# Kernel optimization log

Measured on AMD Instinct MI355X. Metric: run time of the kernel, lower is better.

The kernel has to match this reference:

```python
import jax, jax.numpy as jnp
import numpy as np

L, B, D = 2048, 2, 1024
H, DK, DV = 16, 64, 64
SPAN = 128
LN_EPS = 1e-5


def setup_inputs() -> dict:
    key = jax.random.key(0)
    ks = jax.random.split(key, 8)
    s_qk = np.sqrt(2.0 / (D + DK)).astype(np.float32)
    s_v = np.sqrt(2.0 / (D + DV)).astype(np.float32)
    return {
        "query": jax.random.normal(ks[0], (L, B, D), jnp.float32),
        "key": jax.random.normal(ks[1], (L, B, D), jnp.float32),
        "value": jax.random.normal(ks[2], (L, B, D), jnp.float32),
        "Wq": jax.random.normal(ks[3], (D, H * DK), jnp.float32) * s_qk,
        "bq": jnp.zeros((H * DK,), jnp.float32),
        "Wk": jax.random.normal(ks[4], (D, H * DK), jnp.float32) * s_qk,
        "bk": jnp.zeros((H * DK,), jnp.float32),
        "Wv": jax.random.normal(ks[5], (D, H * DV), jnp.float32) * s_v,
        "bv": jnp.zeros((H * DV,), jnp.float32),
        "Wfc": jax.random.normal(ks[6], (H * DV, D), jnp.float32) * np.sqrt(2.0 / (H * DV + D)).astype(np.float32),
        "bfc": jnp.zeros((D,), jnp.float32),
        "gamma": jnp.ones((D,), jnp.float32),
        "beta": jnp.zeros((D,), jnp.float32),
    }


def reference(query, key, value, Wq, bq, Wk, bk, Wv, bv, Wfc, bfc, gamma, beta):
    l, b, d = query.shape
    # projections: (l,b,H*dk) -> (H,b,l,dk)   [torch rearrange 'l b (head k) -> head b l k']
    q = (query @ Wq + bq).reshape(l, b, H, DK).transpose(2, 1, 0, 3)
    k = (key @ Wk + bk).reshape(l, b, H, DK).transpose(2, 1, 0, 3)
    v = (value @ Wv + bv).reshape(l, b, H, DV).transpose(2, 1, 0, 3)
    scores = jnp.einsum("hblk,hbtk->hblt", q, k) / jnp.sqrt(jnp.float32(DK))
    # banded additive mask: keep |j - i| <= SPAN
    idx = jnp.arange(l)
    band = jnp.abs(idx[None, :] - idx[:, None]) <= SPAN  # (l, l)
    scores = jnp.where(band[None, None], scores, -jnp.inf)
    attn = jax.nn.softmax(scores, axis=-1)
    out = jnp.einsum("hblt,hbtv->hblv", attn, v)
    # 'head b l v -> l b (head v)'
    out = out.transpose(2, 1, 0, 3).reshape(l, b, H * DV)
    out = out @ Wfc + bfc  # dropout p=0.0 -> identity
    y = out + query  # residual
    mu = jnp.mean(y, axis=-1, keepdims=True)
    var = jnp.mean(jnp.square(y - mu), axis=-1, keepdims=True)
    y = (y - mu) * jax.lax.rsqrt(var + LN_EPS) * gamma + beta
    return (y, attn)
```

## Files before the change

### kernel.cpp

```cpp
#include <hip/hip_runtime.h>
#include <stdint.h>

#define L_SEQ 2048
#define BB 2
#define DD 1024
#define NH 16
#define SPAN 128

typedef __attribute__((ext_vector_type(8))) short short8;
typedef __attribute__((ext_vector_type(4))) float floatx4;

__device__ __forceinline__ short f32_bf16(float f) {
  uint32_t u = __float_as_uint(f);
  u += 0x7FFFu + ((u >> 16) & 1u);
  return (short)(u >> 16);
}
__device__ __forceinline__ float bf2f(short s) {
  return __uint_as_float(((uint32_t)(uint16_t)s) << 16);
}

__device__ __forceinline__ void gld16(const short* g, short* l) {
  __builtin_amdgcn_global_load_lds(
      (__attribute__((address_space(1))) void*)(g),
      (__attribute__((address_space(3))) void*)(l), 16, 0, 0);
}

__global__ __launch_bounds__(256) void k_convert(
    const float* __restrict__ s0, const float* __restrict__ s1, const float* __restrict__ s2,
    short* __restrict__ d0, short* __restrict__ d1, short* __restrict__ d2) {
  const float* s = blockIdx.y == 0 ? s0 : (blockIdx.y == 1 ? s1 : s2);
  short* d = blockIdx.y == 0 ? d0 : (blockIdx.y == 1 ? d1 : d2);
  int i = blockIdx.x * 256 + threadIdx.x;
  float4 v = ((const float4*)s)[i];
  short4 o;
  o.x = f32_bf16(v.x); o.y = f32_bf16(v.y); o.z = f32_bf16(v.z); o.w = f32_bf16(v.w);
  ((short4*)d)[i] = o;
}

__global__ __launch_bounds__(256) void k_transpose(
    const float* __restrict__ w0, const float* __restrict__ w1,
    const float* __restrict__ w2, const float* __restrict__ w3,
    short* __restrict__ dst) {
  __shared__ float tile[32][33];
  const float* src = blockIdx.z == 0 ? w0 : blockIdx.z == 1 ? w1 : blockIdx.z == 2 ? w2 : w3;
  short* out = dst + (size_t)blockIdx.z * (DD * DD);
  int bx = blockIdx.x * 32, by = blockIdx.y * 32;
  int tx = threadIdx.x, ty = threadIdx.y;
#pragma unroll
  for (int r = 0; r < 32; r += 8)
    tile[ty + r][tx] = src[(size_t)(by + ty + r) * DD + bx + tx];
  __syncthreads();
#pragma unroll
  for (int r = 0; r < 32; r += 8)
    out[(size_t)(bx + ty + r) * DD + by + tx] = f32_bf16(tile[tx][ty + r]);
}

#define BM 128
#define BN 128
#define BK 32

__device__ __forceinline__ void gemm_core(const short* __restrict__ A,
                                          const short* __restrict__ BT,
                                          floatx4 acc[4][4], int bm0, int bn0) {
  __shared__ short As[BM * BK];
  __shared__ short Bs[BN * BK];
  int tid = threadIdx.x;
  int wave = tid >> 6, lane = tid & 63;
  int li = lane & 15, quad = lane >> 4;
  int wm = (wave & 1) * 64, wn = (wave >> 1) * 64;
  int srow = wave * 32 + (lane >> 2);
  int scol = (lane & 3) * 8;
  const short* gA = A + (size_t)(bm0 + srow) * DD + scol;
  const short* gB = BT + (size_t)(bn0 + srow) * DD + scol;
  short* lA = &As[wave * 32 * BK];
  short* lB = &Bs[wave * 32 * BK];
  for (int k0 = 0; k0 < DD; k0 += BK) {
    __syncthreads();
    gld16(gA + k0, lA);
    gld16(gA + (size_t)16 * DD + k0, lA + 16 * BK);
    gld16(gB + k0, lB);
    gld16(gB + (size_t)16 * DD + k0, lB + 16 * BK);
    __syncthreads();
    short8 af[4], bf[4];
#pragma unroll
    for (int t = 0; t < 4; ++t) {
      af[t] = *(const short8*)&As[(wm + t * 16 + li) * BK + quad * 8];
      bf[t] = *(const short8*)&Bs[(wn + t * 16 + li) * BK + quad * 8];
    }
#pragma unroll
    for (int tm = 0; tm < 4; ++tm)
#pragma unroll
      for (int tn = 0; tn < 4; ++tn)
        acc[tm][tn] = __builtin_amdgcn_mfma_f32_16x16x32_bf16(af[tm], bf[tn], acc[tm][tn], 0, 0, 0);
  }
}

__global__ __launch_bounds__(256) void k_proj(
    const short* __restrict__ xq, const short* __restrict__ xk, const short* __restrict__ xv,
    const short* __restrict__ WT,
    const float* __restrict__ bq, const float* __restrict__ bk, const float* __restrict__ bv,
    short* __restrict__ qo, short* __restrict__ ko, short* __restrict__ vo) {
  int mode = blockIdx.z;
  const short* A = mode == 0 ? xq : (mode == 1 ? xk : xv);
  const short* BT = WT + (size_t)mode * DD * DD;
  const float* bias = mode == 0 ? bq : (mode == 1 ? bk : bv);
  floatx4 acc[4][4] = {};
  int bm0 = blockIdx.y * BM, bn0 = blockIdx.x * BN;
  gemm_core(A, BT, acc, bm0, bn0);

  int tid = threadIdx.x;
  int wave = tid >> 6, lane = tid & 63;
  int li = lane & 15, quad = lane >> 4;
  int wm = (wave & 1) * 64, wn = (wave >> 1) * 64;
  short* dst = (mode == 0) ? qo : (mode == 1 ? ko : vo);
#pragma unroll
  for (int tm = 0; tm < 4; ++tm) {
#pragma unroll
    for (int tn = 0; tn < 4; ++tn) {
      int gn = bn0 + wn + tn * 16 + li;
      float bs = bias[gn];
      int h = gn >> 6, dk = gn & 63;
#pragma unroll
      for (int r = 0; r < 4; ++r) {
        int gm = bm0 + wm + tm * 16 + quad * 4 + r;
        int l = gm >> 1, b = gm & 1;
        dst[(((size_t)h * BB + b) * L_SEQ + l) * 64 + dk] = f32_bf16(acc[tm][tn][r] + bs);
      }
    }
  }
}

__global__ __launch_bounds__(256) void k_vt(const short* __restrict__ vl, short* __restrict__ vt) {
  __shared__ short tl[64][72];
  int l0 = blockIdx.x * 64, hb = blockIdx.y;
  const short* src = vl + ((size_t)hb * L_SEQ + l0) * 64;
  short* dst = vt + (size_t)hb * 64 * L_SEQ + l0;
  int tid = threadIdx.x;
  int r = tid >> 2, c0 = (tid & 3) * 16;
  *(short8*)&tl[r][c0] = *(const short8*)(src + (size_t)r * 64 + c0);
  *(short8*)&tl[r][c0 + 8] = *(const short8*)(src + (size_t)r * 64 + c0 + 8);
  __syncthreads();
  int d = tid >> 2, lb = (tid & 3) * 16;
  short8 o0, o1;
#pragma unroll
  for (int j = 0; j < 8; ++j) o0[j] = tl[lb + j][d];
#pragma unroll
  for (int j = 0; j < 8; ++j) o1[j] = tl[lb + 8 + j][d];
  *(short8*)(dst + (size_t)d * L_SEQ + lb) = o0;
  *(short8*)(dst + (size_t)d * L_SEQ + lb + 8) = o1;
}

__global__ __launch_bounds__(256) void k_attn(
    const short* __restrict__ qw, const short* __restrict__ kw, const short* __restrict__ vTw,
    float* __restrict__ attn_out, short* __restrict__ ctx) {
  __shared__ short P[4][16 * 296];
  const int wv = threadIdx.x >> 6, lane = threadIdx.x & 63;
  const int li = lane & 15, quad = lane >> 4;
  const int i0 = blockIdx.x * 64 + wv * 16;
  const int hb = blockIdx.y;
  const short* Q = qw + (size_t)hb * L_SEQ * 64;
  const short* K = kw + (size_t)hb * L_SEQ * 64;
  const short* VT = vTw + (size_t)hb * 64 * L_SEQ;
  float* Aout = attn_out + (size_t)hb * L_SEQ * L_SEQ;

  short8 qf0 = *(const short8*)(Q + (size_t)(i0 + li) * 64 + quad * 8);
  short8 qf1 = *(const short8*)(Q + (size_t)(i0 + li) * 64 + 32 + quad * 8);

  floatx4 S[17];
  const int jbase = i0 - SPAN;
#pragma unroll
  for (int t = 0; t < 17; ++t) {
    int j0 = jbase + t * 16;
    floatx4 acc = {0.f, 0.f, 0.f, 0.f};
    if (j0 >= 0 && j0 < L_SEQ) {
      const short* kp = K + (size_t)(j0 + li) * 64 + quad * 8;
      short8 kf0 = *(const short8*)kp;
      short8 kf1 = *(const short8*)(kp + 32);
      acc = __builtin_amdgcn_mfma_f32_16x16x32_bf16(qf0, kf0, acc, 0, 0, 0);
      acc = __builtin_amdgcn_mfma_f32_16x16x32_bf16(qf1, kf1, acc, 0, 0, 0);
    }
    S[t] = acc;
  }
  float mrow[4] = {-1e30f, -1e30f, -1e30f, -1e30f};
#pragma unroll
  for (int t = 0; t < 17; ++t) {
    int j0 = jbase + t * 16;
    bool tvalid = (j0 >= 0) && (j0 < L_SEQ);
    int j = j0 + li;
#pragma unroll
    for (int r = 0; r < 4; ++r) {
      int i = i0 + quad * 4 + r;
      bool inband = tvalid && (j >= i - SPAN) && (j <= i + SPAN);
      float s = inband ? S[t][r] * 0.125f : -1e30f;
      S[t][r] = s;
      mrow[r] = fmaxf(mrow[r], s);
    }
  }
#pragma unroll
  for (int m = 1; m <= 8; m <<= 1)
#pragma unroll
    for (int r = 0; r < 4; ++r) mrow[r] = fmaxf(mrow[r], __shfl_xor(mrow[r], m));
  float lsum[4] = {0.f, 0.f, 0.f, 0.f};
#pragma unroll
  for (int t = 0; t < 17; ++t)
#pragma unroll
    for (int r = 0; r < 4; ++r) {
      float p = __expf(S[t][r] - mrow[r]);
      S[t][r] = p;
      lsum[r] += p;
    }
#pragma unroll
  for (int m = 1; m <= 8; m <<= 1)
#pragma unroll
    for (int r = 0; r < 4; ++r) lsum[r] += __shfl_xor(lsum[r], m);
  float inv[4];
#pragma unroll
  for (int r = 0; r < 4; ++r) inv[r] = 1.0f / lsum[r];

  short* myP = P[wv];
#pragma unroll
  for (int t = 0; t < 17; ++t)
#pragma unroll
    for (int r = 0; r < 4; ++r)
      myP[(quad * 4 + r) * 296 + t * 16 + li] = f32_bf16(S[t][r] * inv[r]);
  *(short4*)&myP[(lane >> 2) * 296 + 272 + (lane & 3) * 4] = short4{0, 0, 0, 0};
  __syncthreads();

  floatx4 O[4] = {};
#pragma unroll
  for (int c = 0; c < 9; ++c) {
    short8 pf = *(const short8*)&myP[li * 296 + c * 32 + quad * 8];
    int jg = jbase + c * 32 + quad * 8;
    int jc = (jg >= 0 && jg < L_SEQ) ? jg : 0;
#pragma unroll
    for (int n = 0; n < 4; ++n) {
      short8 vf = *(const short8*)(VT + (size_t)(n * 16 + li) * L_SEQ + jc);
      O[n] = __builtin_amdgcn_mfma_f32_16x16x32_bf16(pf, vf, O[n], 0, 0, 0);
    }
  }
  const int b = hb & 1, h = hb >> 1;
#pragma unroll
  for (int n = 0; n < 4; ++n)
#pragma unroll
    for (int r = 0; r < 4; ++r) {
      int irow = quad * 4 + r;
      ctx[((size_t)(i0 + irow) * BB + b) * DD + h * 64 + n * 16 + li] = f32_bf16(O[n][r]);
    }

#pragma unroll 4
  for (int row = 0; row < 16; ++row) {
    float* orow = Aout + (size_t)(i0 + row) * L_SEQ;
    const short* prow = &myP[row * 296];
#pragma unroll
    for (int it = 0; it < 8; ++it) {
      int col = it * 256 + lane * 4;
      int s = col - jbase;
      float4 v = {0.f, 0.f, 0.f, 0.f};
      if (s >= 0 && s < 288) {
        short4 p4 = *(const short4*)(prow + s);
        v.x = bf2f(p4.x); v.y = bf2f(p4.y); v.z = bf2f(p4.z); v.w = bf2f(p4.w);
      }
      *(float4*)(orow + col) = v;
    }
  }
}

__global__ __launch_bounds__(256) void k_fc(
    const short* __restrict__ ctx, const short* __restrict__ WfcT,
    const float* __restrict__ bfc, const float* __restrict__ query,
    float* __restrict__ ypre) {
  floatx4 acc[4][4] = {};
  int bm0 = blockIdx.y * BM, bn0 = blockIdx.x * BN;
  gemm_core(ctx, WfcT, acc, bm0, bn0);
  int tid = threadIdx.x;
  int wave = tid >> 6, lane = tid & 63;
  int li = lane & 15, quad = lane >> 4;
  int wm = (wave & 1) * 64, wn = (wave >> 1) * 64;
#pragma unroll
  for (int tm = 0; tm < 4; ++tm)
#pragma unroll
    for (int tn = 0; tn < 4; ++tn) {
      int gn = bn0 + wn + tn * 16 + li;
      float bs = bfc[gn];
#pragma unroll
      for (int r = 0; r < 4; ++r) {
        int gm = bm0 + wm + tm * 16 + quad * 4 + r;
        ypre[(size_t)gm * DD + gn] = acc[tm][tn][r] + bs + query[(size_t)gm * DD + gn];
      }
    }
}

__global__ __launch_bounds__(256) void k_ln(
    const float* __restrict__ yp, const float* __restrict__ gamma,
    const float* __restrict__ beta, float* __restrict__ out) {
  __shared__ float red[8];
  int row = blockIdx.x, tid = threadIdx.x;
  float4 v = ((const float4*)(yp + (size_t)row * DD))[tid];
  float s = v.x + v.y + v.z + v.w;
  float s2 = v.x * v.x + v.y * v.y + v.z * v.z + v.w * v.w;
#pragma unroll
  for (int m = 1; m <= 32; m <<= 1) {
    s += __shfl_xor(s, m);
    s2 += __shfl_xor(s2, m);
  }
  int wv = tid >> 6;
  if ((tid & 63) == 0) { red[wv] = s; red[wv + 4] = s2; }
  __syncthreads();
  s = red[0] + red[1] + red[2] + red[3];
  s2 = red[4] + red[5] + red[6] + red[7];
  float mu = s * (1.0f / DD);
  float var = s2 * (1.0f / DD) - mu * mu;
  float rs = rsqrtf(var + 1e-5f);
  float4 g = ((const float4*)gamma)[tid];
  float4 bb = ((const float4*)beta)[tid];
  float4 o;
  o.x = (v.x - mu) * rs * g.x + bb.x;
  o.y = (v.y - mu) * rs * g.y + bb.y;
  o.z = (v.z - mu) * rs * g.z + bb.z;
  o.w = (v.w - mu) * rs * g.w + bb.w;
  ((float4*)(out + (size_t)row * DD))[tid] = o;
}

extern "C" void kernel_launch(void* const* d_in, const int* in_sizes, int n_in,
                              void* d_out, int out_size, void* d_ws, size_t ws_size,
                              hipStream_t stream) {
  const float* query = (const float*)d_in[0];
  const float* key   = (const float*)d_in[1];
  const float* value = (const float*)d_in[2];
  const float* Wq    = (const float*)d_in[3];
  const float* bq    = (const float*)d_in[4];
  const float* Wk    = (const float*)d_in[5];
  const float* bk    = (const float*)d_in[6];
  const float* Wv    = (const float*)d_in[7];
  const float* bv    = (const float*)d_in[8];
  const float* Wfc   = (const float*)d_in[9];
  const float* bfc   = (const float*)d_in[10];
  const float* gamma = (const float*)d_in[11];
  const float* beta  = (const float*)d_in[12];
  float* out = (float*)d_out;
  float* attn = out + (size_t)L_SEQ * BB * DD;

  char* w = (char*)d_ws;
  short* xq_b  = (short*)(w);
  short* xk_b  = (short*)(w + ((size_t)8 << 20));
  short* xv_b  = (short*)(w + ((size_t)16 << 20));
  short* WT    = (short*)(w + ((size_t)24 << 20));
  short* q_ws  = (short*)(w + ((size_t)32 << 20));
  short* k_ws  = (short*)(w + ((size_t)40 << 20));
  short* v_lin = (short*)(w + ((size_t)48 << 20));
  short* vT_ws = (short*)(w + ((size_t)56 << 20));
  short* ctx   = (short*)(w + ((size_t)64 << 20));
  float* ypre  = (float*)(w + ((size_t)72 << 20));

  k_convert<<<dim3(4096, 3), 256, 0, stream>>>(query, key, value, xq_b, xk_b, xv_b);
  k_transpose<<<dim3(32, 32, 4), dim3(32, 8), 0, stream>>>(Wq, Wk, Wv, Wfc, WT);
  k_proj<<<dim3(8, 32, 3), 256, 0, stream>>>(xq_b, xk_b, xv_b, WT, bq, bk, bv, q_ws, k_ws, v_lin);
  k_vt<<<dim3(32, 32), 256, 0, stream>>>(v_lin, vT_ws);
  k_attn<<<dim3(32, 32), 256, 0, stream>>>(q_ws, k_ws, vT_ws, attn, ctx);
  k_fc<<<dim3(8, 32), 256, 0, stream>>>(ctx, WT + (size_t)3 * DD * DD, bfc, query, ypre);
  k_ln<<<4096, 256, 0, stream>>>(ypre, gamma, beta, out);
}
```

Baseline: 720.1 us.

## Merge prep kernels, stage K in LDS, widen GEMM K-step, nontemporal attn stores

Fuses the input conversion and weight transpose into one launch, and doubles the GEMM K-step to 64 so each iteration issues more loads and MFMAs between barriers. The attention kernel now stages the block's shared K window in LDS once, instead of each wave reading K from global memory, and reuses that buffer for P. The 128 MB attention-matrix writes use nontemporal stores to avoid polluting the cache. The cost is more LDS per block and an extra barrier, which may lower occupancy.

```diff
diff --git a/kernel.cpp b/kernel.cpp
--- a/kernel.cpp
+++ b/kernel.cpp
@@ -25,67 +25,87 @@
       (__attribute__((address_space(3))) void*)(l), 16, 0, 0);
 }
 
-__global__ __launch_bounds__(256) void k_convert(
+__global__ __launch_bounds__(256) void k_prep(
     const float* __restrict__ s0, const float* __restrict__ s1, const float* __restrict__ s2,
-    short* __restrict__ d0, short* __restrict__ d1, short* __restrict__ d2) {
-  const float* s = blockIdx.y == 0 ? s0 : (blockIdx.y == 1 ? s1 : s2);
-  short* d = blockIdx.y == 0 ? d0 : (blockIdx.y == 1 ? d1 : d2);
-  int i = blockIdx.x * 256 + threadIdx.x;
-  float4 v = ((const float4*)s)[i];
-  short4 o;
-  o.x = f32_bf16(v.x); o.y = f32_bf16(v.y); o.z = f32_bf16(v.z); o.w = f32_bf16(v.w);
-  ((short4*)d)[i] = o;
-}
-
-__global__ __launch_bounds__(256) void k_transpose(
     const float* __restrict__ w0, const float* __restrict__ w1,
     const float* __restrict__ w2, const float* __restrict__ w3,
-    short* __restrict__ dst) {
+    short* __restrict__ d0, short* __restrict__ d1, short* __restrict__ d2,
+    short* __restrict__ WT) {
   __shared__ float tile[32][33];
-  const float* src = blockIdx.z == 0 ? w0 : blockIdx.z == 1 ? w1 : blockIdx.z == 2 ? w2 : w3;
-  short* out = dst + (size_t)blockIdx.z * (DD * DD);
-  int bx = blockIdx.x * 32, by = blockIdx.y * 32;
-  int tx = threadIdx.x, ty = threadIdx.y;
-#pragma unroll
-  for (int r = 0; r < 32; r += 8)
-    tile[ty + r][tx] = src[(size_t)(by + ty + r) * DD + bx + tx];
-  __syncthreads();
-#pragma unroll
-  for (int r = 0; r < 32; r += 8)
-    out[(size_t)(bx + ty + r) * DD + by + tx] = f32_bf16(tile[tx][ty + r]);
+  int bid = blockIdx.x, tid = threadIdx.x;
+  if (bid < 12288) {
+    int y = bid >> 12;
+    const float* s = y == 0 ? s0 : (y == 1 ? s1 : s2);
+    short* d = y == 0 ? d0 : (y == 1 ? d1 : d2);
+    int i = (bid & 4095) * 256 + tid;
+    float4 v = ((const float4*)s)[i];
+    short4 o;
+    o.x = f32_bf16(v.x); o.y = f32_bf16(v.y); o.z = f32_bf16(v.z); o.w = f32_bf16(v.w);
+    ((short4*)d)[i] = o;
+  } else {
+    int b2 = bid - 12288;
+    int z = b2 >> 10;
+    int xy = b2 & 1023;
+    int bx = (xy & 31) * 32, by = (xy >> 5) * 32;
+    int tx = tid & 31, ty = tid >> 5;
+    const float* src = z == 0 ? w0 : z == 1 ? w1 : z == 2 ? w2 : w3;
+    short* out = WT + (size_t)z * (DD * DD);
+#pragma unroll
+    for (int r = 0; r < 32; r += 8)
+      tile[ty + r][tx] = src[(size_t)(by + ty + r) * DD + bx + tx];
+    __syncthreads();
+#pragma unroll
+    for (int r = 0; r < 32; r += 8)
+      out[(size_t)(bx + ty + r) * DD + by + tx] = f32_bf16(tile[tx][ty + r]);
+  }
 }
 
 #define BM 128
 #define BN 128
-#define BK 32
 
 __device__ __forceinline__ void gemm_core(const short* __restrict__ A,
                                           const short* __restrict__ BT,
                                           floatx4 acc[4][4], int bm0, int bn0) {
-  __shared__ short As[BM * BK];
-  __shared__ short Bs[BN * BK];
+  __shared__ short As0[BM * 32], As1[BM * 32];
+  __shared__ short Bs0[BN * 32], Bs1[BN * 32];
   int tid = threadIdx.x;
   int wave = tid >> 6, lane = tid & 63;
   int li = lane & 15, quad = lane >> 4;
   int wm = (wave & 1) * 64, wn = (wave >> 1) * 64;
-  int srow = wave * 32 + (lane >> 2);
-  int scol = (lane & 3) * 8;
-  const short* gA = A + (size_t)(bm0 + srow) * DD + scol;
-  const short* gB = BT + (size_t)(bn0 + srow) * DD + scol;
-  short* lA = &As[wave * 32 * BK];
-  short* lB = &Bs[wave * 32 * BK];
-  for (int k0 = 0; k0 < DD; k0 += BK) {
+  int r0 = wave * 32 + (lane >> 2);
+  int c0 = (lane & 3) * 8;
+  const short* gA = A + (size_t)(bm0 + r0) * DD + c0;
+  const short* gB = BT + (size_t)(bn0 + r0) * DD + c0;
+  short* lA0 = &As0[wave * 32 * 32];
+  short* lA1 = &As1[wave * 32 * 32];
+  short* lB0 = &Bs0[wave * 32 * 32];
+  short* lB1 = &Bs1[wave * 32 * 32];
+  for (int k0 = 0; k0 < DD; k0 += 64) {
     __syncthreads();
-    gld16(gA + k0, lA);
-    gld16(gA + (size_t)16 * DD + k0, lA + 16 * BK);
-    gld16(gB + k0, lB);
-    gld16(gB + (size_t)16 * DD + k0, lB + 16 * BK);
+    gld16(gA + k0, lA0);
+    gld16(gA + (size_t)16 * DD + k0, lA0 + 16 * 32);
+    gld16(gA + k0 + 32, lA1);
+    gld16(gA + (size_t)16 * DD + k0 + 32, lA1 + 16 * 32);
+    gld16(gB + k0, lB0);
+    gld16(gB + (size_t)16 * DD + k0, lB0 + 16 * 32);
+    gld16(gB + k0 + 32, lB1);
+    gld16(gB + (size_t)16 * DD + k0 + 32, lB1 + 16 * 32);
     __syncthreads();
     short8 af[4], bf[4];
 #pragma unroll
     for (int t = 0; t < 4; ++t) {
-      af[t] = *(const short8*)&As[(wm + t * 16 + li) * BK + quad * 8];
-      bf[t] = *(const short8*)&Bs[(wn + t * 16 + li) * BK + quad * 8];
+      af[t] = *(const short8*)&As0[(wm + t * 16 + li) * 32 + quad * 8];
+      bf[t] = *(const short8*)&Bs0[(wn + t * 16 + li) * 32 + quad * 8];
+    }
+#pragma unroll
+    for (int tm = 0; tm < 4; ++tm)
+#pragma unroll
+      for (int tn = 0; tn < 4; ++tn)
+        acc[tm][tn] = __builtin_amdgcn_mfma_f32_16x16x32_bf16(af[tm], bf[tn], acc[tm][tn], 0, 0, 0);
+#pragma unroll
+    for (int t = 0; t < 4; ++t) {
+      af[t] = *(const short8*)&As1[(wm + t * 16 + li) * 32 + quad * 8];
+      bf[t] = *(const short8*)&Bs1[(wn + t * 16 + li) * 32 + quad * 8];
     }
 #pragma unroll
     for (int tm = 0; tm < 4; ++tm)
@@ -153,18 +173,37 @@
 __global__ __launch_bounds__(256) void k_attn(
     const short* __restrict__ qw, const short* __restrict__ kw, const short* __restrict__ vTw,
     float* __restrict__ attn_out, short* __restrict__ ctx) {
-  __shared__ short P[4][16 * 296];
-  const int wv = threadIdx.x >> 6, lane = threadIdx.x & 63;
+  __shared__ short sbuf[20480];
+  short* K0 = sbuf;
+  short* K1 = sbuf + 10240;
+  const int tid = threadIdx.x;
+  const int wv = tid >> 6, lane = tid & 63;
   const int li = lane & 15, quad = lane >> 4;
-  const int i0 = blockIdx.x * 64 + wv * 16;
+  const int i0b = blockIdx.x * 64;
+  const int i0 = i0b + wv * 16;
+  const int jb = i0b - SPAN;
   const int hb = blockIdx.y;
   const short* Q = qw + (size_t)hb * L_SEQ * 64;
   const short* K = kw + (size_t)hb * L_SEQ * 64;
   const short* VT = vTw + (size_t)hb * 64 * L_SEQ;
   float* Aout = attn_out + (size_t)hb * L_SEQ * L_SEQ;
 
+#pragma unroll
+  for (int t = 0; t < 10; ++t) {
+    int idx = wv + 4 * t;
+    int half = idx >= 20 ? 1 : 0;
+    int ridx = idx - half * 20;
+    int row = ridx * 16 + (lane >> 2);
+    int jr = jb + row;
+    int jc = jr < 0 ? 0 : (jr >= L_SEQ ? L_SEQ - 1 : jr);
+    const short* g = K + (size_t)jc * 64 + half * 32 + (lane & 3) * 8;
+    short* l = (half ? K1 : K0) + ridx * 16 * 32;
+    gld16(g, l);
+  }
+
   short8 qf0 = *(const short8*)(Q + (size_t)(i0 + li) * 64 + quad * 8);
   short8 qf1 = *(const short8*)(Q + (size_t)(i0 + li) * 64 + 32 + quad * 8);
+  __syncthreads();
 
   floatx4 S[17];
   const int jbase = i0 - SPAN;
@@ -172,10 +211,10 @@
   for (int t = 0; t < 17; ++t) {
     int j0 = jbase + t * 16;
     floatx4 acc = {0.f, 0.f, 0.f, 0.f};
-    if (j0 >= 0 && j0 < L_SEQ) {
-      const short* kp = K + (size_t)(j0 + li) * 64 + quad * 8;
-      short8 kf0 = *(const short8*)kp;
-      short8 kf1 = *(const short8*)(kp + 32);
+    if (j0 > -16 && j0 < L_SEQ) {
+      int jrel = (wv + t) * 16;
+      short8 kf0 = *(const short8*)&K0[(jrel + li) * 32 + quad * 8];
+      short8 kf1 = *(const short8*)&K1[(jrel + li) * 32 + quad * 8];
       acc = __builtin_amdgcn_mfma_f32_16x16x32_bf16(qf0, kf0, acc, 0, 0, 0);
       acc = __builtin_amdgcn_mfma_f32_16x16x32_bf16(qf1, kf1, acc, 0, 0, 0);
     }
@@ -184,13 +223,11 @@
   float mrow[4] = {-1e30f, -1e30f, -1e30f, -1e30f};
 #pragma unroll
   for (int t = 0; t < 17; ++t) {
-    int j0 = jbase + t * 16;
-    bool tvalid = (j0 >= 0) && (j0 < L_SEQ);
-    int j = j0 + li;
+    int j = jbase + t * 16 + li;
 #pragma unroll
     for (int r = 0; r < 4; ++r) {
       int i = i0 + quad * 4 + r;
-      bool inband = tvalid && (j >= i - SPAN) && (j <= i + SPAN);
+      bool inband = (j >= i - SPAN) && (j <= i + SPAN) && (j >= 0) && (j < L_SEQ);
       float s = inband ? S[t][r] * 0.125f : -1e30f;
       S[t][r] = s;
       mrow[r] = fmaxf(mrow[r], s);
@@ -217,7 +254,8 @@
 #pragma unroll
   for (int r = 0; r < 4; ++r) inv[r] = 1.0f / lsum[r];
 
-  short* myP = P[wv];
+  __syncthreads();
+  short* myP = sbuf + wv * 4736;
 #pragma unroll
   for (int t = 0; t < 17; ++t)
 #pragma unroll
@@ -255,12 +293,12 @@
     for (int it = 0; it < 8; ++it) {
       int col = it * 256 + lane * 4;
       int s = col - jbase;
-      float4 v = {0.f, 0.f, 0.f, 0.f};
+      floatx4 v = {0.f, 0.f, 0.f, 0.f};
       if (s >= 0 && s < 288) {
         short4 p4 = *(const short4*)(prow + s);
         v.x = bf2f(p4.x); v.y = bf2f(p4.y); v.z = bf2f(p4.z); v.w = bf2f(p4.w);
       }
-      *(float4*)(orow + col) = v;
+      __builtin_nontemporal_store(v, (floatx4*)(orow + col));
     }
   }
 }
@@ -352,8 +390,8 @@
   short* ctx   = (short*)(w + ((size_t)64 << 20));
   float* ypre  = (float*)(w + ((size_t)72 << 20));
 
-  k_convert<<<dim3(4096, 3), 256, 0, stream>>>(query, key, value, xq_b, xk_b, xv_b);
-  k_transpose<<<dim3(32, 32, 4), dim3(32, 8), 0, stream>>>(Wq, Wk, Wv, Wfc, WT);
+  k_prep<<<16384, 256, 0, stream>>>(query, key, value, Wq, Wk, Wv, Wfc,
+                                    xq_b, xk_b, xv_b, WT);
   k_proj<<<dim3(8, 32, 3), 256, 0, stream>>>(xq_b, xk_b, xv_b, WT, bq, bk, bv, q_ws, k_ws, v_lin);
   k_vt<<<dim3(32, 32), 256, 0, stream>>>(v_lin, vT_ws);
   k_attn<<<dim3(32, 32), 256, 0, stream>>>(q_ws, k_ws, vT_ws, attn, ctx);
```

Result: no change. 706.9 us (-1.8%).
